# Performance work log

Hardware: AMD Instinct MI355X
Metric: run time of the kernel (lower is better)

Reference implementation:

```python
import jax, jax.numpy as jnp
import numpy as np

NEG_SLOPE = 0.2  # PyG GATConv default LeakyReLU slope
EPS = 1e-16


def gat_conv(x, src, dst, W, att_src, att_dst, bias, concat):
    """One GATConv layer (PyG semantics, self-loops already in src/dst).
    x: [N, Fin]; src/dst: [E'] int; W: [Fin, H*C]; att_*: [H, C]; bias: [H*C] or [C].
    """
    N = x.shape[0]
    H, C = att_src.shape
    h = (x @ W).reshape(N, H, C)                      # [N, H, C]
    a_s = jnp.einsum('nhc,hc->nh', h, att_src)        # [N, H]
    a_d = jnp.einsum('nhc,hc->nh', h, att_dst)        # [N, H]
    logits = jax.nn.leaky_relu(a_s[src] + a_d[dst], NEG_SLOPE)  # [E', H]
    # segment softmax over incoming edges of each destination node
    m = jax.ops.segment_max(logits, dst, num_segments=N)        # [N, H]
    m = jnp.where(jnp.isfinite(m), m, 0.0)
    e = jnp.exp(logits - m[dst])                                # [E', H]
    denom = jax.ops.segment_sum(e, dst, num_segments=N)         # [N, H]
    alpha = e / (denom[dst] + EPS)                              # [E', H]
    msg = h[src] * alpha[:, :, None]                            # [E', H, C]
    out = jax.ops.segment_sum(msg, dst, num_segments=N)         # [N, H, C]
    out = out.reshape(N, H * C) if concat else out.mean(axis=1)
    return out + bias


def setup_inputs() -> dict:
    key = jax.random.key(0)
    ks = jax.random.split(key, 8)
    N, E, IN, HID, OUT, H1 = 50000, 800000, 128, 64, 32, 2
    x = jax.random.normal(ks[0], (N, IN), dtype=jnp.float32)
    edge_index = jax.random.randint(ks[1], (2, E), 0, N, dtype=jnp.int32)
    # glorot-ish scaled params
    W1 = jax.random.normal(ks[2], (IN, H1 * HID), dtype=jnp.float32) * (1.0 / np.sqrt(IN))
    att_src1 = jax.random.normal(ks[3], (H1, HID), dtype=jnp.float32) * (1.0 / np.sqrt(HID))
    att_dst1 = jax.random.normal(ks[4], (H1, HID), dtype=jnp.float32) * (1.0 / np.sqrt(HID))
    bias1 = jnp.zeros((H1 * HID,), dtype=jnp.float32)
    W2 = jax.random.normal(ks[5], (H1 * HID, OUT), dtype=jnp.float32) * (1.0 / np.sqrt(H1 * HID))
    att_src2 = jax.random.normal(ks[6], (1, OUT), dtype=jnp.float32) * (1.0 / np.sqrt(OUT))
    att_dst2 = jax.random.normal(ks[7], (1, OUT), dtype=jnp.float32) * (1.0 / np.sqrt(OUT))
    bias2 = jnp.zeros((OUT,), dtype=jnp.float32)
    return {"x": x, "edge_index": edge_index, "W1": W1, "att_src1": att_src1,
            "att_dst1": att_dst1, "bias1": bias1, "W2": W2, "att_src2": att_src2,
            "att_dst2": att_dst2, "bias2": bias2}


def reference(x, edge_index, W1, att_src1, att_dst1, bias1, W2, att_src2, att_dst2, bias2):
    N = x.shape[0]
    loops = jnp.arange(N, dtype=edge_index.dtype)
    src = jnp.concatenate([edge_index[0], loops])   # add self loops (PyG default)
    dst = jnp.concatenate([edge_index[1], loops])
    h = gat_conv(x, src, dst, W1, att_src1, att_dst1, bias1, concat=True)
    h = jax.nn.relu(h)
    out = gat_conv(h, src, dst, W2, att_src2, att_dst2, bias2, concat=False)
    return out
```

## Files before the change

### kernel.cpp

```cpp
#include <hip/hip_runtime.h>
#include <hip/hip_bf16.h>
#include <math.h>


__device__ __forceinline__ float lrelu(float x) { return x > 0.f ? x : 0.2f * x; }

__device__ __forceinline__ float2 bf2_unpack(unsigned u) {
  return make_float2(__uint_as_float(u << 16), __uint_as_float(u & 0xffff0000u));
}

__device__ __forceinline__ float readlane_f(float v, int l) {
  return __uint_as_float((unsigned)__builtin_amdgcn_readlane(__float_as_uint(v), l));
}

constexpr int CAP = 5632;

__global__ void k_partition(const int* __restrict__ srcA, const int* __restrict__ dstA,
                            int E, int Nn, int* __restrict__ gcnt,
                            unsigned* __restrict__ bkt) {
  __shared__ int hist[256];
  __shared__ int bbase[256];
  const int NBK = (Nn + 255) >> 8;
  const int tid = threadIdx.x;
  for (int i = tid; i < 256; i += 512) hist[i] = 0;
  __syncthreads();
  const int tot = E + Nn;
  const int g0 = blockIdx.x * 4096;
  unsigned pk[8]; int bk[8], rk[8]; int cnt = 0;
#pragma unroll
  for (int j = 0; j < 8; ++j) {
    int g = g0 + j * 512 + tid;
    if (g >= tot) break;
    int s, d;
    if (g < E) { s = srcA[g]; d = dstA[g]; } else { s = g - E; d = s; }
    int b = d >> 8;
    pk[cnt] = (unsigned)s | ((unsigned)(d & 255) << 16);
    bk[cnt] = b;
    rk[cnt] = atomicAdd(&hist[b], 1);
    cnt++;
  }
  __syncthreads();
  for (int i = tid; i < 256; i += 512) {
    int h = (i < NBK) ? hist[i] : 0;
    bbase[i] = h ? atomicAdd(&gcnt[i], h) : 0;
  }
  __syncthreads();
  for (int j = 0; j < cnt; ++j) {
    int pos = bbase[bk[j]] + rk[j];
    if (pos < CAP) bkt[(size_t)bk[j] * CAP + pos] = pk[j];
  }
}

__global__ void k_bscan(const int* __restrict__ gcnt, int* __restrict__ bstart,
                        int NBK, int* __restrict__ offsN, int tot) {
  int lane = threadIdx.x;
  int carry = 0;
  for (int c = 0; c < NBK; c += 64) {
    int idx = c + lane;
    int v = (idx < NBK) ? gcnt[idx] : 0;
    int x = v;
#pragma unroll
    for (int o = 1; o < 64; o <<= 1) { int t = __shfl_up(x, o); if (lane >= o) x += t; }
    if (idx < NBK) bstart[idx] = carry + x - v;
    carry += __shfl(x, 63);
  }
  if (lane == 0) { bstart[NBK] = carry; *offsN = tot; }
}

__global__ void k_fine(const unsigned* __restrict__ bkt, const int* __restrict__ gcnt,
                       const int* __restrict__ bstart, int Nn,
                       int* __restrict__ offs, unsigned* __restrict__ csr) {
  __shared__ int fc[256];
  __shared__ int lo[256];
  __shared__ int cur[256];
  const int b = blockIdx.x;
  const int tid = threadIdx.x;
  int m = gcnt[b]; if (m > CAP) m = CAP;
  const unsigned* p = bkt + (size_t)b * CAP;
  for (int i = tid; i < 256; i += 512) fc[i] = 0;
  __syncthreads();
  for (int i = tid; i < m; i += 512) atomicAdd(&fc[p[i] >> 16], 1);
  __syncthreads();
  if (tid < 64) {
    int carry = 0;
    for (int c = 0; c < 256; c += 64) {
      int v = fc[c + tid]; int x = v;
#pragma unroll
      for (int o = 1; o < 64; o <<= 1) { int t = __shfl_up(x, o); if (tid >= o) x += t; }
      lo[c + tid] = carry + x - v;
      carry += __shfl(x, 63);
    }
  }
  __syncthreads();
  const int base = bstart[b];
  for (int i = tid; i < 256; i += 512) {
    cur[i] = lo[i];
    int n = (b << 8) + i;
    if (n < Nn) offs[n] = base + lo[i];
  }
  __syncthreads();
  const unsigned hi = (unsigned)(b << 8) << 16;
  for (int i = tid; i < m; i += 512) {
    unsigned e = p[i];
    int pos = atomicAdd(&cur[e >> 16], 1);
    csr[base + pos] = (hi | (e >> 16 << 16)) | (e & 0xffffu);
  }
}

__global__ void k_wts1(const unsigned* __restrict__ csr, const float* __restrict__ as1,
                       const float* __restrict__ ad1, float2* __restrict__ w, int tot) {
  int i = blockIdx.x * 256 + threadIdx.x;
  if (i >= tot) return;
  unsigned e = csr[i];
  int s = e & 0xffffu, d = e >> 16;
  float2 a = ((const float2*)as1)[s];
  float2 b = ((const float2*)ad1)[d];
  w[i] = make_float2(__expf(lrelu(a.x + b.x)), __expf(lrelu(a.y + b.y)));
}

__global__ void k_wts2(const unsigned* __restrict__ csr, const float* __restrict__ as2,
                       const float* __restrict__ ad2, float* __restrict__ w, int tot) {
  int i = blockIdx.x * 256 + threadIdx.x;
  if (i >= tot) return;
  unsigned e = csr[i];
  int s = e & 0xffffu, d = e >> 16;
  w[i] = __expf(lrelu(as2[s] + ad2[d]));
}

template <int BM, int BN, int BK, int TM, int TN, int HS>
__global__ void k_gemm_att(const float* __restrict__ A, const float* __restrict__ B,
                           __hip_bfloat16* __restrict__ Cb,
                           const float* __restrict__ attS, const float* __restrict__ attD,
                           float* __restrict__ asO, float* __restrict__ adO,
                           int M, int K, int N) {
  static_assert(BN / TN == 16, "epilogue reduce assumes 16 tx lanes");
  __shared__ float As[BK][BM + 4];
  __shared__ float Bs[BK][BN + 4];
  const int NT = (BM / TM) * (BN / TN);
  const int tid = threadIdx.x;
  const int tx = tid % 16;
  const int ty = tid / 16;
  const int row0 = blockIdx.x * BM;
  const int head = blockIdx.y;
  const int col0 = head * BN;

  float acc[TM][TN];
#pragma unroll
  for (int i = 0; i < TM; i++)
#pragma unroll
    for (int j = 0; j < TN; j++) acc[i][j] = 0.f;

  for (int k0 = 0; k0 < K; k0 += BK) {
#pragma unroll
    for (int q = tid; q < BM * (BK / 4); q += NT) {
      int row = q / (BK / 4), kq = (q % (BK / 4)) << 2;
      int gm = row0 + row;
      float4 v = make_float4(0.f, 0.f, 0.f, 0.f);
      if (gm < M) v = *(const float4*)(A + (size_t)gm * K + k0 + kq);
      As[kq + 0][row] = v.x; As[kq + 1][row] = v.y;
      As[kq + 2][row] = v.z; As[kq + 3][row] = v.w;
    }
#pragma unroll
    for (int q = tid; q < BK * (BN / 4); q += NT) {
      int krow = q / (BN / 4), nq = (q % (BN / 4)) << 2;
      float4 v = *(const float4*)(B + (size_t)(k0 + krow) * N + col0 + nq);
      *(float4*)&Bs[krow][nq] = v;
    }
    __syncthreads();
#pragma unroll
    for (int k = 0; k < BK; ++k) {
      float a[TM], b[TN];
      *(float4*)&a[0] = *(const float4*)&As[k][ty * TM];
      if constexpr (TN == 4) *(float4*)&b[0] = *(const float4*)&Bs[k][tx * TN];
      else                   *(float2*)&b[0] = *(const float2*)&Bs[k][tx * TN];
#pragma unroll
      for (int i = 0; i < TM; i++)
#pragma unroll
        for (int j = 0; j < TN; j++) acc[i][j] += a[i] * b[j];
    }
    __syncthreads();
  }

  float atS[TN], atD[TN];
#pragma unroll
  for (int j = 0; j < TN; j++) {
    atS[j] = attS[col0 + tx * TN + j];
    atD[j] = attD[col0 + tx * TN + j];
  }
#pragma unroll
  for (int i = 0; i < TM; i++) {
    int gm = row0 + ty * TM + i;
    float ps = 0.f, pd = 0.f;
#pragma unroll
    for (int j = 0; j < TN; j++) { ps += acc[i][j] * atS[j]; pd += acc[i][j] * atD[j]; }
#pragma unroll
    for (int off = 1; off < 16; off <<= 1) { ps += __shfl_xor(ps, off); pd += __shfl_xor(pd, off); }
    if (gm < M) {
      if (tx == 0) { asO[(size_t)gm * HS + head] = ps; adO[(size_t)gm * HS + head] = pd; }
      union { __hip_bfloat16 h[TN]; unsigned u[TN / 2]; } pkk;
#pragma unroll
      for (int j = 0; j < TN; j++) pkk.h[j] = __float2bfloat16(acc[i][j]);
      if constexpr (TN == 4) *(uint2*)(Cb + (size_t)gm * N + col0 + tx * TN) = *(uint2*)pkk.u;
      else                   *(unsigned*)(Cb + (size_t)gm * N + col0 + tx * TN) = pkk.u[0];
    }
  }
}

__global__ void k_agg1(const unsigned* __restrict__ h1b, const float2* __restrict__ w,
                       const unsigned* __restrict__ csr, const int* __restrict__ offs,
                       const float* __restrict__ bias, float* __restrict__ out, int Nn) {
  int n = blockIdx.x * (blockDim.x >> 6) + (threadIdx.x >> 6);
  if (n >= Nn) return;
  int lane = threadIdx.x & 63;
  int head = lane >> 5;
  int beg = offs[n], end = offs[n + 1];
  float ax = 0.f, ay = 0.f, den = 0.f;
  int i = beg;
  while (i < end) {
    int m = end - i; if (m > 64) m = 64;
    int idx = i + lane;
    bool ok = idx < end;
    float2 wv = ok ? w[idx] : make_float2(0.f, 0.f);
    int sv = ok ? (int)(csr[idx] & 0xffffu) : 0;
    float wsel = head ? wv.y : wv.x;
    int j = 0;
    for (; j + 4 <= m; j += 4) {
#pragma unroll
      for (int u = 0; u < 4; ++u) {
        int s = __builtin_amdgcn_readlane(sv, j + u);
        float e = readlane_f(wsel, j + u);
        float ex = readlane_f(wv.x, j + u);
        float ey = readlane_f(wv.y, j + u);
        e = head ? ey : ex;
        float2 v = bf2_unpack(h1b[(size_t)s * 64 + lane]);
        ax += e * v.x; ay += e * v.y; den += e;
      }
    }
    for (; j < m; ++j) {
      int s = __builtin_amdgcn_readlane(sv, j);
      float ex = readlane_f(wv.x, j);
      float ey = readlane_f(wv.y, j);
      float e = head ? ey : ex;
      float2 v = bf2_unpack(h1b[(size_t)s * 64 + lane]);
      ax += e * v.x; ay += e * v.y; den += e;
    }
    i += m;
  }
  float inv = 1.f / (den + 1e-16f);
  const float2 bv = ((const float2*)bias)[lane];
  float o0 = ax * inv + bv.x; o0 = o0 > 0.f ? o0 : 0.f;
  float o1 = ay * inv + bv.y; o1 = o1 > 0.f ? o1 : 0.f;
  ((float2*)out)[(size_t)n * 64 + lane] = make_float2(o0, o1);
}

__global__ void k_agg2(const unsigned* __restrict__ h2b, const float* __restrict__ w,
                       const unsigned* __restrict__ csr, const int* __restrict__ offs,
                       const float* __restrict__ bias, float* __restrict__ out, int Nn) {
  int n = blockIdx.x * (blockDim.x >> 6) + (threadIdx.x >> 6);
  if (n >= Nn) return;
  int lane = threadIdx.x & 63;
  int g = lane >> 4, cp = lane & 15;
  int beg = offs[n], end = offs[n + 1];
  float ax = 0.f, ay = 0.f, den = 0.f;
  int i = beg;
  while (i < end) {
    int m = end - i; if (m > 64) m = 64;
    int idx = i + lane;
    bool okl = idx < end;
    float wv = okl ? w[idx] : 0.f;
    int sv = okl ? (int)(csr[idx] & 0xffffu) : 0;
    for (int j = 0; j < m; j += 4) {
      int jj = j + g;
      float e = __shfl(wv, jj);
      int s = __shfl(sv, jj);
      float2 v = bf2_unpack(h2b[(size_t)s * 16 + cp]);
      ax += e * v.x; ay += e * v.y; den += e;
    }
    i += m;
  }
  ax += __shfl_xor(ax, 16); ay += __shfl_xor(ay, 16); den += __shfl_xor(den, 16);
  ax += __shfl_xor(ax, 32); ay += __shfl_xor(ay, 32); den += __shfl_xor(den, 32);
  if (lane < 16) {
    float inv = 1.f / (den + 1e-16f);
    const float2 bv = ((const float2*)bias)[cp];
    ((float2*)out)[(size_t)n * 16 + cp] =
        make_float2(ax * inv + bv.x, ay * inv + bv.y);
  }
}

extern "C" void kernel_launch(void* const* d_in, const int* in_sizes, int n_in,
                              void* d_out, int out_size, void* d_ws, size_t ws_size,
                              hipStream_t stream) {
  const float* x      = (const float*)d_in[0];
  const int*   ei     = (const int*)d_in[1];
  const float* W1     = (const float*)d_in[2];
  const float* att_s1 = (const float*)d_in[3];
  const float* att_d1 = (const float*)d_in[4];
  const float* bias1  = (const float*)d_in[5];
  const float* W2     = (const float*)d_in[6];
  const float* att_s2 = (const float*)d_in[7];
  const float* att_d2 = (const float*)d_in[8];
  const float* bias2  = (const float*)d_in[9];
  float* out = (float*)d_out;

  const int N = in_sizes[0] / 128;
  const int E = in_sizes[1] / 2;
  const int* srcA = ei;
  const int* dstA = ei + E;
  const int tot = E + N;
  const int NBK = (N + 255) >> 8;

  char* w = (char*)d_ws;
  auto alloc = [&](size_t bytes) { char* p = w; w += (bytes + 255) / 256 * 256; return p; };
  __hip_bfloat16* h1b = (__hip_bfloat16*)alloc((size_t)N * 128 * 2);
  __hip_bfloat16* h2b = (__hip_bfloat16*)alloc((size_t)N * 32 * 2);
  float* h2in   = (float*)alloc((size_t)N * 128 * 4);
  float* as1    = (float*)alloc((size_t)N * 2 * 4);
  float* ad1    = (float*)alloc((size_t)N * 2 * 4);
  float* as2    = (float*)alloc((size_t)N * 4);
  float* ad2    = (float*)alloc((size_t)N * 4);
  float2* wt1   = (float2*)alloc((size_t)tot * 8);
  float* wt2    = (float*)alloc((size_t)tot * 4);
  int*   gcnt   = (int*)alloc((size_t)NBK * 4);
  int*   bstart = (int*)alloc((size_t)(NBK + 1) * 4);
  unsigned* bkt = (unsigned*)alloc((size_t)NBK * CAP * 4);
  int*   offs   = (int*)alloc((size_t)(N + 1) * 4);
  unsigned* csr = (unsigned*)alloc((size_t)tot * 4);

  hipMemsetAsync(gcnt, 0, (size_t)NBK * 4, stream);
  k_partition<<<(tot + 4095) / 4096, 512, 0, stream>>>(srcA, dstA, E, N, gcnt, bkt);
  k_bscan<<<1, 64, 0, stream>>>(gcnt, bstart, NBK, offs + N, tot);
  k_fine<<<NBK, 512, 0, stream>>>(bkt, gcnt, bstart, N, offs, csr);

  dim3 g1((N + 63) / 64, 2);
  k_gemm_att<64, 64, 16, 4, 4, 2><<<g1, 256, 0, stream>>>(
      x, W1, h1b, att_s1, att_d1, as1, ad1, N, 128, 128);
  int ebw = (tot + 255) / 256;
  k_wts1<<<ebw, 256, 0, stream>>>(csr, as1, ad1, wt1, tot);
  int nb = (N + 3) / 4;
  k_agg1<<<nb, 256, 0, stream>>>((const unsigned*)h1b, wt1, csr, offs, bias1, h2in, N);

  dim3 g2((N + 63) / 64, 1);
  k_gemm_att<64, 32, 16, 4, 2, 1><<<g2, 256, 0, stream>>>(
      h2in, W2, h2b, att_s2, att_d2, as2, ad2, N, 128, 32);
  k_wts2<<<ebw, 256, 0, stream>>>(csr, as2, ad2, wt2, tot);
  k_agg2<<<nb, 256, 0, stream>>>((const unsigned*)h2b, wt2, csr, offs, bias2, out, N);
}
```

Measured before the change: 221.0 us.

## Use MFMA bf16 GEMMs, fuse edge weights into aggregation, drop scan kernel

```diff
diff --git a/kernel.cpp b/kernel.cpp
--- a/kernel.cpp
+++ b/kernel.cpp
@@ -1,20 +1,26 @@
 #include <hip/hip_runtime.h>
-#include <hip/hip_bf16.h>
 #include <math.h>
 
 
+typedef __bf16 bf16x8 __attribute__((ext_vector_type(8)));
+typedef float f32x4 __attribute__((ext_vector_type(4)));
+
 __device__ __forceinline__ float lrelu(float x) { return x > 0.f ? x : 0.2f * x; }
 
+__device__ __forceinline__ unsigned short f2bf(float x) {
+  unsigned u = __float_as_uint(x);
+  return (unsigned short)((u + 0x7fffu + ((u >> 16) & 1u)) >> 16);
+}
 __device__ __forceinline__ float2 bf2_unpack(unsigned u) {
   return make_float2(__uint_as_float(u << 16), __uint_as_float(u & 0xffff0000u));
 }
-
 __device__ __forceinline__ float readlane_f(float v, int l) {
   return __uint_as_float((unsigned)__builtin_amdgcn_readlane(__float_as_uint(v), l));
 }
 
 constexpr int CAP = 5632;
 
+__launch_bounds__(512)
 __global__ void k_partition(const int* __restrict__ srcA, const int* __restrict__ dstA,
                             int E, int Nn, int* __restrict__ gcnt,
                             unsigned* __restrict__ bkt) {
@@ -51,37 +57,28 @@
   }
 }
 
-__global__ void k_bscan(const int* __restrict__ gcnt, int* __restrict__ bstart,
-                        int NBK, int* __restrict__ offsN, int tot) {
-  int lane = threadIdx.x;
-  int carry = 0;
-  for (int c = 0; c < NBK; c += 64) {
-    int idx = c + lane;
-    int v = (idx < NBK) ? gcnt[idx] : 0;
-    int x = v;
-#pragma unroll
-    for (int o = 1; o < 64; o <<= 1) { int t = __shfl_up(x, o); if (lane >= o) x += t; }
-    if (idx < NBK) bstart[idx] = carry + x - v;
-    carry += __shfl(x, 63);
-  }
-  if (lane == 0) { bstart[NBK] = carry; *offsN = tot; }
-}
-
+__launch_bounds__(512)
 __global__ void k_fine(const unsigned* __restrict__ bkt, const int* __restrict__ gcnt,
-                       const int* __restrict__ bstart, int Nn,
-                       int* __restrict__ offs, unsigned* __restrict__ csr) {
+                       int Nn, int tot, int* __restrict__ offs, unsigned* __restrict__ csr) {
   __shared__ int fc[256];
   __shared__ int lo[256];
   __shared__ int cur[256];
+  __shared__ int baseS;
   const int b = blockIdx.x;
   const int tid = threadIdx.x;
   int m = gcnt[b]; if (m > CAP) m = CAP;
   const unsigned* p = bkt + (size_t)b * CAP;
+  if (b == 0 && tid == 0) offs[Nn] = tot;
   for (int i = tid; i < 256; i += 512) fc[i] = 0;
   __syncthreads();
   for (int i = tid; i < m; i += 512) atomicAdd(&fc[p[i] >> 16], 1);
   __syncthreads();
   if (tid < 64) {
+    int s = 0;
+    for (int c = tid; c < b; c += 64) s += gcnt[c];
+#pragma unroll
+    for (int o = 32; o; o >>= 1) s += __shfl_xor(s, o);
+    if (tid == 0) baseS = s;
     int carry = 0;
     for (int c = 0; c < 256; c += 64) {
       int v = fc[c + tid]; int x = v;
@@ -92,157 +89,228 @@
     }
   }
   __syncthreads();
-  const int base = bstart[b];
+  const int base = baseS;
   for (int i = tid; i < 256; i += 512) {
     cur[i] = lo[i];
     int n = (b << 8) + i;
     if (n < Nn) offs[n] = base + lo[i];
   }
   __syncthreads();
-  const unsigned hi = (unsigned)(b << 8) << 16;
+  const unsigned hi = ((unsigned)b) << 24;
   for (int i = tid; i < m; i += 512) {
     unsigned e = p[i];
     int pos = atomicAdd(&cur[e >> 16], 1);
-    csr[base + pos] = (hi | (e >> 16 << 16)) | (e & 0xffffu);
-  }
-}
-
-__global__ void k_wts1(const unsigned* __restrict__ csr, const float* __restrict__ as1,
-                       const float* __restrict__ ad1, float2* __restrict__ w, int tot) {
-  int i = blockIdx.x * 256 + threadIdx.x;
-  if (i >= tot) return;
-  unsigned e = csr[i];
-  int s = e & 0xffffu, d = e >> 16;
-  float2 a = ((const float2*)as1)[s];
-  float2 b = ((const float2*)ad1)[d];
-  w[i] = make_float2(__expf(lrelu(a.x + b.x)), __expf(lrelu(a.y + b.y)));
-}
-
-__global__ void k_wts2(const unsigned* __restrict__ csr, const float* __restrict__ as2,
-                       const float* __restrict__ ad2, float* __restrict__ w, int tot) {
-  int i = blockIdx.x * 256 + threadIdx.x;
-  if (i >= tot) return;
-  unsigned e = csr[i];
-  int s = e & 0xffffu, d = e >> 16;
-  w[i] = __expf(lrelu(as2[s] + ad2[d]));
-}
-
-template <int BM, int BN, int BK, int TM, int TN, int HS>
-__global__ void k_gemm_att(const float* __restrict__ A, const float* __restrict__ B,
-                           __hip_bfloat16* __restrict__ Cb,
-                           const float* __restrict__ attS, const float* __restrict__ attD,
-                           float* __restrict__ asO, float* __restrict__ adO,
-                           int M, int K, int N) {
-  static_assert(BN / TN == 16, "epilogue reduce assumes 16 tx lanes");
-  __shared__ float As[BK][BM + 4];
-  __shared__ float Bs[BK][BN + 4];
-  const int NT = (BM / TM) * (BN / TN);
+    csr[base + pos] = hi | ((e >> 16) << 16) | (e & 0xffffu);
+  }
+}
+
+__launch_bounds__(256)
+__global__ void k_gemm1(const float* __restrict__ A, const float* __restrict__ B,
+                        unsigned short* __restrict__ Cb,
+                        const float* __restrict__ attS, const float* __restrict__ attD,
+                        float* __restrict__ asO, float* __restrict__ adO, int M) {
+  __shared__ union { unsigned short bl[32 * 64 * 8]; float accl[64 * 132]; } sm;
   const int tid = threadIdx.x;
-  const int tx = tid % 16;
-  const int ty = tid / 16;
-  const int row0 = blockIdx.x * BM;
-  const int head = blockIdx.y;
-  const int col0 = head * BN;
-
-  float acc[TM][TN];
-#pragma unroll
-  for (int i = 0; i < TM; i++)
-#pragma unroll
-    for (int j = 0; j < TN; j++) acc[i][j] = 0.f;
-
-  for (int k0 = 0; k0 < K; k0 += BK) {
-#pragma unroll
-    for (int q = tid; q < BM * (BK / 4); q += NT) {
-      int row = q / (BK / 4), kq = (q % (BK / 4)) << 2;
-      int gm = row0 + row;
-      float4 v = make_float4(0.f, 0.f, 0.f, 0.f);
-      if (gm < M) v = *(const float4*)(A + (size_t)gm * K + k0 + kq);
-      As[kq + 0][row] = v.x; As[kq + 1][row] = v.y;
-      As[kq + 2][row] = v.z; As[kq + 3][row] = v.w;
-    }
-#pragma unroll
-    for (int q = tid; q < BK * (BN / 4); q += NT) {
-      int krow = q / (BN / 4), nq = (q % (BN / 4)) << 2;
-      float4 v = *(const float4*)(B + (size_t)(k0 + krow) * N + col0 + nq);
-      *(float4*)&Bs[krow][nq] = v;
-    }
-    __syncthreads();
-#pragma unroll
-    for (int k = 0; k < BK; ++k) {
-      float a[TM], b[TN];
-      *(float4*)&a[0] = *(const float4*)&As[k][ty * TM];
-      if constexpr (TN == 4) *(float4*)&b[0] = *(const float4*)&Bs[k][tx * TN];
-      else                   *(float2*)&b[0] = *(const float2*)&Bs[k][tx * TN];
-#pragma unroll
-      for (int i = 0; i < TM; i++)
-#pragma unroll
-        for (int j = 0; j < TN; j++) acc[i][j] += a[i] * b[j];
-    }
-    __syncthreads();
-  }
-
-  float atS[TN], atD[TN];
-#pragma unroll
-  for (int j = 0; j < TN; j++) {
-    atS[j] = attS[col0 + tx * TN + j];
-    atD[j] = attD[col0 + tx * TN + j];
-  }
-#pragma unroll
-  for (int i = 0; i < TM; i++) {
-    int gm = row0 + ty * TM + i;
+  const int lane = tid & 63, w = tid >> 6;
+  const int row0 = blockIdx.x * 64;
+  for (int i = tid; i < 128 * 32; i += 256) {
+    int k = i >> 5, n4 = (i & 31) << 2;
+    float4 v = *(const float4*)(B + k * 128 + n4);
+    int c = k >> 5, q = (k >> 3) & 3, j = k & 7;
+    float vv[4] = {v.x, v.y, v.z, v.w};
+#pragma unroll
+    for (int u2 = 0; u2 < 4; ++u2) {
+      int n = n4 + u2, t = n >> 4, l = q * 16 + (n & 15);
+      sm.bl[((t * 4 + c) * 64 + l) * 8 + j] = f2bf(vv[u2]);
+    }
+  }
+  int mrow = row0 + 16 * w + (lane & 15);
+  bool rok = mrow < M;
+  const int q = lane >> 4;
+  bf16x8 afr[4];
+  union { unsigned short s[8]; bf16x8 b; } cv;
+#pragma unroll
+  for (int c = 0; c < 4; ++c) {
+    float4 u0 = make_float4(0.f, 0.f, 0.f, 0.f), u1 = u0;
+    if (rok) {
+      const float* ap = A + (size_t)mrow * 128 + c * 32 + q * 8;
+      u0 = *(const float4*)ap; u1 = *(const float4*)(ap + 4);
+    }
+    cv.s[0] = f2bf(u0.x); cv.s[1] = f2bf(u0.y); cv.s[2] = f2bf(u0.z); cv.s[3] = f2bf(u0.w);
+    cv.s[4] = f2bf(u1.x); cv.s[5] = f2bf(u1.y); cv.s[6] = f2bf(u1.z); cv.s[7] = f2bf(u1.w);
+    afr[c] = cv.b;
+  }
+  __syncthreads();
+  f32x4 acc[8];
+#pragma unroll
+  for (int t = 0; t < 8; ++t) {
+    f32x4 a = {0.f, 0.f, 0.f, 0.f};
+#pragma unroll
+    for (int c = 0; c < 4; ++c) {
+      bf16x8 bf = *(((const bf16x8*)sm.bl) + (t * 4 + c) * 64 + lane);
+      a = __builtin_amdgcn_mfma_f32_16x16x32_bf16(afr[c], bf, a, 0, 0, 0);
+    }
+    acc[t] = a;
+  }
+  __syncthreads();
+  {
+    int rbase = 16 * w + q * 4, cl = lane & 15;
+#pragma unroll
+    for (int t = 0; t < 8; ++t)
+#pragma unroll
+      for (int r = 0; r < 4; ++r)
+        sm.accl[(rbase + r) * 132 + 16 * t + cl] = acc[t][r];
+  }
+  __syncthreads();
+  {
+    int row = tid >> 2, cg = tid & 3, c0 = cg * 32;
+    int grow = row0 + row;
+    const float* ar = &sm.accl[row * 132 + c0];
     float ps = 0.f, pd = 0.f;
-#pragma unroll
-    for (int j = 0; j < TN; j++) { ps += acc[i][j] * atS[j]; pd += acc[i][j] * atD[j]; }
-#pragma unroll
-    for (int off = 1; off < 16; off <<= 1) { ps += __shfl_xor(ps, off); pd += __shfl_xor(pd, off); }
-    if (gm < M) {
-      if (tx == 0) { asO[(size_t)gm * HS + head] = ps; adO[(size_t)gm * HS + head] = pd; }
-      union { __hip_bfloat16 h[TN]; unsigned u[TN / 2]; } pkk;
-#pragma unroll
-      for (int j = 0; j < TN; j++) pkk.h[j] = __float2bfloat16(acc[i][j]);
-      if constexpr (TN == 4) *(uint2*)(Cb + (size_t)gm * N + col0 + tx * TN) = *(uint2*)pkk.u;
-      else                   *(unsigned*)(Cb + (size_t)gm * N + col0 + tx * TN) = pkk.u[0];
-    }
-  }
-}
-
-__global__ void k_agg1(const unsigned* __restrict__ h1b, const float2* __restrict__ w,
-                       const unsigned* __restrict__ csr, const int* __restrict__ offs,
-                       const float* __restrict__ bias, float* __restrict__ out, int Nn) {
+    unsigned pkv[16];
+#pragma unroll
+    for (int u2 = 0; u2 < 8; ++u2) {
+      float4 v  = *(const float4*)(ar + u2 * 4);
+      float4 s4 = *(const float4*)(attS + c0 + u2 * 4);
+      float4 d4 = *(const float4*)(attD + c0 + u2 * 4);
+      ps += v.x * s4.x + v.y * s4.y + v.z * s4.z + v.w * s4.w;
+      pd += v.x * d4.x + v.y * d4.y + v.z * d4.z + v.w * d4.w;
+      pkv[u2 * 2]     = (unsigned)f2bf(v.x) | ((unsigned)f2bf(v.y) << 16);
+      pkv[u2 * 2 + 1] = (unsigned)f2bf(v.z) | ((unsigned)f2bf(v.w) << 16);
+    }
+    ps += __shfl_xor(ps, 1); pd += __shfl_xor(pd, 1);
+    if (grow < M) {
+      if ((tid & 1) == 0) {
+        int head = (tid >> 1) & 1;
+        asO[(size_t)grow * 2 + head] = ps; adO[(size_t)grow * 2 + head] = pd;
+      }
+      unsigned* cp = (unsigned*)(Cb + (size_t)grow * 128 + c0);
+      *(uint4*)(cp)      = make_uint4(pkv[0], pkv[1], pkv[2], pkv[3]);
+      *(uint4*)(cp + 4)  = make_uint4(pkv[4], pkv[5], pkv[6], pkv[7]);
+      *(uint4*)(cp + 8)  = make_uint4(pkv[8], pkv[9], pkv[10], pkv[11]);
+      *(uint4*)(cp + 12) = make_uint4(pkv[12], pkv[13], pkv[14], pkv[15]);
+    }
+  }
+}
+
+__launch_bounds__(256)
+__global__ void k_gemm2(const unsigned* __restrict__ Ab, const float* __restrict__ B,
+                        unsigned short* __restrict__ Cb,
+                        const float* __restrict__ attS, const float* __restrict__ attD,
+                        float* __restrict__ asO, float* __restrict__ adO, int M) {
+  __shared__ unsigned short bl[8 * 64 * 8];
+  __shared__ float accl[64 * 36];
+  const int tid = threadIdx.x;
+  const int lane = tid & 63, w = tid >> 6;
+  const int row0 = blockIdx.x * 64;
+  for (int i = tid; i < 128 * 8; i += 256) {
+    int k = i >> 3, n4 = (i & 7) << 2;
+    float4 v = *(const float4*)(B + k * 32 + n4);
+    int c = k >> 5, q = (k >> 3) & 3, j = k & 7;
+    float vv[4] = {v.x, v.y, v.z, v.w};
+#pragma unroll
+    for (int u2 = 0; u2 < 4; ++u2) {
+      int n = n4 + u2, t = n >> 4, l = q * 16 + (n & 15);
+      bl[((t * 4 + c) * 64 + l) * 8 + j] = f2bf(vv[u2]);
+    }
+  }
+  int mrow = row0 + 16 * w + (lane & 15);
+  bool rok = mrow < M;
+  const int q = lane >> 4;
+  bf16x8 afr[4];
+#pragma unroll
+  for (int c = 0; c < 4; ++c) {
+    uint4 u = make_uint4(0u, 0u, 0u, 0u);
+    if (rok) u = *(const uint4*)(Ab + (size_t)mrow * 64 + c * 16 + q * 4);
+    afr[c] = __builtin_bit_cast(bf16x8, u);
+  }
+  __syncthreads();
+  f32x4 acc[2];
+#pragma unroll
+  for (int t = 0; t < 2; ++t) {
+    f32x4 a = {0.f, 0.f, 0.f, 0.f};
+#pragma unroll
+    for (int c = 0; c < 4; ++c) {
+      bf16x8 bf = *(((const bf16x8*)bl) + (t * 4 + c) * 64 + lane);
+      a = __builtin_amdgcn_mfma_f32_16x16x32_bf16(afr[c], bf, a, 0, 0, 0);
+    }
+    acc[t] = a;
+  }
+  {
+    int rbase = 16 * w + q * 4, cl = lane & 15;
+#pragma unroll
+    for (int t = 0; t < 2; ++t)
+#pragma unroll
+      for (int r = 0; r < 4; ++r)
+        accl[(rbase + r) * 36 + 16 * t + cl] = acc[t][r];
+  }
+  __syncthreads();
+  {
+    int row = tid >> 2, cg = tid & 3, c0 = cg * 8;
+    int grow = row0 + row;
+    const float* ar = &accl[row * 36 + c0];
+    float ps = 0.f, pd = 0.f;
+    unsigned pk[4];
+#pragma unroll
+    for (int u2 = 0; u2 < 2; ++u2) {
+      float4 v  = *(const float4*)(ar + u2 * 4);
+      float4 s4 = *(const float4*)(attS + c0 + u2 * 4);
+      float4 d4 = *(const float4*)(attD + c0 + u2 * 4);
+      ps += v.x * s4.x + v.y * s4.y + v.z * s4.z + v.w * s4.w;
+      pd += v.x * d4.x + v.y * d4.y + v.z * d4.z + v.w * d4.w;
+      pk[u2 * 2]     = (unsigned)f2bf(v.x) | ((unsigned)f2bf(v.y) << 16);
+      pk[u2 * 2 + 1] = (unsigned)f2bf(v.z) | ((unsigned)f2bf(v.w) << 16);
+    }
+    ps += __shfl_xor(ps, 1); ps += __shfl_xor(ps, 2);
+    pd += __shfl_xor(pd, 1); pd += __shfl_xor(pd, 2);
+    if (grow < M) {
+      if (cg == 0) { asO[grow] = ps; adO[grow] = pd; }
+      *(uint4*)(Cb + (size_t)grow * 32 + c0) = make_uint4(pk[0], pk[1], pk[2], pk[3]);
+    }
+  }
+}
+
+__global__ void k_agg1(const unsigned* __restrict__ h1b, const float* __restrict__ as1,
+                       const float* __restrict__ ad1, const int* __restrict__ offs,
+                       const unsigned* __restrict__ csr, const float* __restrict__ bias,
+                       unsigned* __restrict__ outb, int Nn) {
   int n = blockIdx.x * (blockDim.x >> 6) + (threadIdx.x >> 6);
   if (n >= Nn) return;
   int lane = threadIdx.x & 63;
   int head = lane >> 5;
   int beg = offs[n], end = offs[n + 1];
+  float2 adn = ((const float2*)ad1)[n];
   float ax = 0.f, ay = 0.f, den = 0.f;
   int i = beg;
   while (i < end) {
     int m = end - i; if (m > 64) m = 64;
     int idx = i + lane;
     bool ok = idx < end;
-    float2 wv = ok ? w[idx] : make_float2(0.f, 0.f);
-    int sv = ok ? (int)(csr[idx] & 0xffffu) : 0;
-    float wsel = head ? wv.y : wv.x;
+    unsigned e = ok ? csr[idx] : 0u;
+    int sv = (int)(e & 0xffffu);
+    float w0 = 0.f, w1 = 0.f;
+    if (ok) {
+      float2 a = ((const float2*)as1)[sv];
+      w0 = __expf(lrelu(a.x + adn.x));
+      w1 = __expf(lrelu(a.y + adn.y));
+    }
     int j = 0;
     for (; j + 4 <= m; j += 4) {
 #pragma unroll
       for (int u = 0; u < 4; ++u) {
         int s = __builtin_amdgcn_readlane(sv, j + u);
-        float e = readlane_f(wsel, j + u);
-        float ex = readlane_f(wv.x, j + u);
-        float ey = readlane_f(wv.y, j + u);
-        e = head ? ey : ex;
+        float ex = readlane_f(w0, j + u), ey = readlane_f(w1, j + u);
+        float ee = head ? ey : ex;
         float2 v = bf2_unpack(h1b[(size_t)s * 64 + lane]);
-        ax += e * v.x; ay += e * v.y; den += e;
+        ax += ee * v.x; ay += ee * v.y; den += ee;
       }
     }
     for (; j < m; ++j) {
       int s = __builtin_amdgcn_readlane(sv, j);
-      float ex = readlane_f(wv.x, j);
-      float ey = readlane_f(wv.y, j);
-      float e = head ? ey : ex;
+      float ex = readlane_f(w0, j), ey = readlane_f(w1, j);
+      float ee = head ? ey : ex;
       float2 v = bf2_unpack(h1b[(size_t)s * 64 + lane]);
-      ax += e * v.x; ay += e * v.y; den += e;
+      ax += ee * v.x; ay += ee * v.y; den += ee;
     }
     i += m;
   }
@@ -250,31 +318,34 @@
   const float2 bv = ((const float2*)bias)[lane];
   float o0 = ax * inv + bv.x; o0 = o0 > 0.f ? o0 : 0.f;
   float o1 = ay * inv + bv.y; o1 = o1 > 0.f ? o1 : 0.f;
-  ((float2*)out)[(size_t)n * 64 + lane] = make_float2(o0, o1);
-}
-
-__global__ void k_agg2(const unsigned* __restrict__ h2b, const float* __restrict__ w,
-                       const unsigned* __restrict__ csr, const int* __restrict__ offs,
-                       const float* __restrict__ bias, float* __restrict__ out, int Nn) {
+  outb[(size_t)n * 64 + lane] = (unsigned)f2bf(o0) | ((unsigned)f2bf(o1) << 16);
+}
+
+__global__ void k_agg2(const unsigned* __restrict__ h2b, const float* __restrict__ as2,
+                       const float* __restrict__ ad2, const int* __restrict__ offs,
+                       const unsigned* __restrict__ csr, const float* __restrict__ bias,
+                       float* __restrict__ out, int Nn) {
   int n = blockIdx.x * (blockDim.x >> 6) + (threadIdx.x >> 6);
   if (n >= Nn) return;
   int lane = threadIdx.x & 63;
   int g = lane >> 4, cp = lane & 15;
   int beg = offs[n], end = offs[n + 1];
+  float adn = ad2[n];
   float ax = 0.f, ay = 0.f, den = 0.f;
   int i = beg;
   while (i < end) {
     int m = end - i; if (m > 64) m = 64;
     int idx = i + lane;
-    bool okl = idx < end;
-    float wv = okl ? w[idx] : 0.f;
-    int sv = okl ? (int)(csr[idx] & 0xffffu) : 0;
+    bool ok = idx < end;
+    unsigned e = ok ? csr[idx] : 0u;
+    int sv = (int)(e & 0xffffu);
+    float wv = ok ? __expf(lrelu(as2[sv] + adn)) : 0.f;
     for (int j = 0; j < m; j += 4) {
       int jj = j + g;
-      float e = __shfl(wv, jj);
+      float ee = __shfl(wv, jj);
       int s = __shfl(sv, jj);
       float2 v = bf2_unpack(h2b[(size_t)s * 16 + cp]);
-      ax += e * v.x; ay += e * v.y; den += e;
+      ax += ee * v.x; ay += ee * v.y; den += ee;
     }
     i += m;
   }
@@ -312,37 +383,27 @@
 
   char* w = (char*)d_ws;
   auto alloc = [&](size_t bytes) { char* p = w; w += (bytes + 255) / 256 * 256; return p; };
-  __hip_bfloat16* h1b = (__hip_bfloat16*)alloc((size_t)N * 128 * 2);
-  __hip_bfloat16* h2b = (__hip_bfloat16*)alloc((size_t)N * 32 * 2);
-  float* h2in   = (float*)alloc((size_t)N * 128 * 4);
+  unsigned short* h1b = (unsigned short*)alloc((size_t)N * 128 * 2);
+  unsigned* h2in_b    = (unsigned*)alloc((size_t)N * 64 * 4);
+  unsigned short* h2b = (unsigned short*)alloc((size_t)N * 32 * 2);
   float* as1    = (float*)alloc((size_t)N * 2 * 4);
   float* ad1    = (float*)alloc((size_t)N * 2 * 4);
   float* as2    = (float*)alloc((size_t)N * 4);
   float* ad2    = (float*)alloc((size_t)N * 4);
-  float2* wt1   = (float2*)alloc((size_t)tot * 8);
-  float* wt2    = (float*)alloc((size_t)tot * 4);
   int*   gcnt   = (int*)alloc((size_t)NBK * 4);
-  int*   bstart = (int*)alloc((size_t)(NBK + 1) * 4);
   unsigned* bkt = (unsigned*)alloc((size_t)NBK * CAP * 4);
   int*   offs   = (int*)alloc((size_t)(N + 1) * 4);
   unsigned* csr = (unsigned*)alloc((size_t)tot * 4);
 
   hipMemsetAsync(gcnt, 0, (size_t)NBK * 4, stream);
   k_partition<<<(tot + 4095) / 4096, 512, 0, stream>>>(srcA, dstA, E, N, gcnt, bkt);
-  k_bscan<<<1, 64, 0, stream>>>(gcnt, bstart, NBK, offs + N, tot);
-  k_fine<<<NBK, 512, 0, stream>>>(bkt, gcnt, bstart, N, offs, csr);
-
-  dim3 g1((N + 63) / 64, 2);
-  k_gemm_att<64, 64, 16, 4, 4, 2><<<g1, 256, 0, stream>>>(
-      x, W1, h1b, att_s1, att_d1, as1, ad1, N, 128, 128);
-  int ebw = (tot + 255) / 256;
-  k_wts1<<<ebw, 256, 0, stream>>>(csr, as1, ad1, wt1, tot);
+  k_fine<<<NBK, 512, 0, stream>>>(bkt, gcnt, N, tot, offs, csr);
+
+  int gb = (N + 63) / 64;
+  k_gemm1<<<gb, 256, 0, stream>>>(x, W1, h1b, att_s1, att_d1, as1, ad1, N);
   int nb = (N + 3) / 4;
-  k_agg1<<<nb, 256, 0, stream>>>((const unsigned*)h1b, wt1, csr, offs, bias1, h2in, N);
-
-  dim3 g2((N + 63) / 64, 1);
-  k_gemm_att<64, 32, 16, 4, 2, 1><<<g2, 256, 0, stream>>>(
-      h2in, W2, h2b, att_s2, att_d2, as2, ad2, N, 128, 32);
-  k_wts2<<<ebw, 256, 0, stream>>>(csr, as2, ad2, wt2, tot);
-  k_agg2<<<nb, 256, 0, stream>>>((const unsigned*)h2b, wt2, csr, offs, bias2, out, N);
-}
+  k_agg1<<<nb, 256, 0, stream>>>((const unsigned*)h1b, as1, ad1, offs, csr, bias1, h2in_b, N);
+
+  k_gemm2<<<gb, 256, 0, stream>>>(h2in_b, W2, h2b, att_s2, att_d2, as2, ad2, N);
+  k_agg2<<<nb, 256, 0, stream>>>((const unsigned*)h2b, as2, ad2, offs, csr, bias2, out, N);
+}
```

Result: faster. 203.2 us (-8.1%).
